# Performance work log

Measured on AMD Instinct MI355X. Metric: run time of the kernel, lower is better.

Reference implementation:

```python
import jax, jax.numpy as jnp
import numpy as np

B, T, D, H = 8, 2048, 1024, 128


def setup_inputs() -> dict:
    key = jax.random.key(0)
    k1, k2, k3, k4 = jax.random.split(key, 4)
    x = jax.random.normal(k1, (B, T, D), dtype=jnp.float32)
    # nn.Linear(D, H, bias=False): y = x @ W.T with W [H, D]; we store W as [D, H]
    Wq = jax.random.normal(k2, (D, H), dtype=jnp.float32) * (1.0 / np.sqrt(D))
    Wk = jax.random.normal(k3, (D, H), dtype=jnp.float32) * (1.0 / np.sqrt(D))
    Wv = jax.random.normal(k4, (D, H), dtype=jnp.float32) * (1.0 / np.sqrt(D))
    return {"x": x, "Wq": Wq, "Wk": Wk, "Wv": Wv}


def reference(x, Wq, Wk, Wv):
    # q, k, v projections (bias-free)
    q = jnp.einsum("btd,dh->bth", x, Wq)
    k = jnp.einsum("btd,dh->bth", x, Wk)
    v = jnp.einsum("btd,dh->bth", x, Wv)
    scale = 1.0 / jnp.sqrt(jnp.asarray(q.shape[-1], dtype=q.dtype))
    # full T x T score matrix, as in the original module
    scores = jnp.einsum("bqh,bkh->bqk", q, k) * scale
    T_ = x.shape[1]
    causal = jnp.tril(jnp.ones((T_, T_), dtype=bool))
    scores = jnp.where(causal[None, :, :], scores, -jnp.inf)
    weights = jax.nn.softmax(scores, axis=-1)
    # dropout is identity in eval mode (deterministic reference)
    return jnp.einsum("bqk,bkh->bqh", weights, v)
```

## Files before the change

kernel.cpp:

```cpp
#include <hip/hip_runtime.h>

typedef float  f32x4  __attribute__((ext_vector_type(4)));
typedef __bf16 bf16x8 __attribute__((ext_vector_type(8)));
typedef unsigned short u16;
typedef unsigned int   u32;
typedef u32 u32x4 __attribute__((ext_vector_type(4)));
typedef u16 u16x4 __attribute__((ext_vector_type(4)));
typedef u16 u16x8 __attribute__((ext_vector_type(8)));
typedef float f32x4v __attribute__((ext_vector_type(4)));

#define B_ 8
#define T_ 2048
#define D_ 1024
#define H_ 128
#define M_ (B_ * T_)

__device__ __forceinline__ u16 f2b(float f) {
  u32 u = __builtin_bit_cast(u32, f);
  u32 r = u + 0x7fffu + ((u >> 16) & 1u);
  return (u16)(r >> 16);
}

__device__ __forceinline__ void gl2lds16(const void* g, void* l) {
  __builtin_amdgcn_global_load_lds(
      (const __attribute__((address_space(1))) void*)g,
      (__attribute__((address_space(3))) void*)l, 16, 0, 0);
}

__global__ __launch_bounds__(256) void wt_kernel(const float* __restrict__ Wq,
                                                 const float* __restrict__ Wk,
                                                 const float* __restrict__ Wv,
                                                 u16* __restrict__ ws) {
  __shared__ u16 Ld[32 * 136];
  const float* W = (blockIdx.y == 0) ? Wq : (blockIdx.y == 1) ? Wk : Wv;
  u16* Wt = ws + (size_t)blockIdx.y * (D_ * H_);
  const int d0 = blockIdx.x * 32;
  const int t = threadIdx.x;
  for (int i = 0; i < 4; ++i) {
    int idx = i * 256 + t;
    int d = idx >> 5, h4 = (idx & 31) * 4;
    f32x4v wv = *(const f32x4v*)(W + (size_t)(d0 + d) * H_ + h4);
    u16x4 bv;
    bv[0] = f2b(wv[0]); bv[1] = f2b(wv[1]); bv[2] = f2b(wv[2]); bv[3] = f2b(wv[3]);
    *(u16x4*)(&Ld[d * 136 + h4]) = bv;
  }
  __syncthreads();
  for (int i = 0; i < 2; ++i) {
    int idx = i * 256 + t;
    int h = idx >> 2, d8 = (idx & 3) * 8;
    u16x8 ov;
    for (int j = 0; j < 8; ++j) ov[j] = Ld[(d8 + j) * 136 + h];
    *(u16x8*)(Wt + (size_t)h * D_ + d0 + d8) = ov;
  }
}

__global__ __launch_bounds__(512, 4) void qkv_gemm(const float* __restrict__ x,
                                                   const u16* __restrict__ Wt_all,
                                                   u16* __restrict__ Qb,
                                                   u16* __restrict__ Kb,
                                                   u16* __restrict__ Vt) {
  __shared__ __attribute__((aligned(16))) u16 As[2][64 * 72];
  __shared__ __attribute__((aligned(16))) u16 Bs[2][192 * 64];
  const int m0 = (int)(blockIdx.x >> 1) * 64;
  const int n0 = (int)(blockIdx.x & 1) * 192;
  const int t = threadIdx.x;
  const int lane = t & 63;
  const int w = t >> 6;
  const int wm = (w & 1) * 32, wn = (w >> 1) * 48;
  const int li = lane & 15, q4 = lane >> 4;
  const int arow = t >> 3, ac0 = (t & 7) * 4;
  const int brr = lane >> 3, bp = lane & 7;

  f32x4 acc[2][3];
  for (int i = 0; i < 2; ++i)
    for (int j = 0; j < 3; ++j) acc[i][j] = (f32x4){0.f, 0.f, 0.f, 0.f};

  f32x4v areg[2];
  auto load_a = [&](int kt) {
    for (int ii = 0; ii < 2; ++ii)
      areg[ii] = *(const f32x4v*)(x + (size_t)(m0 + arow) * D_ + kt * 64 + ac0 + ii * 32);
  };
  auto stage_b = [&](int kt, int sb) {
    for (int s3 = 0; s3 < 3; ++s3) {
      int seg = s3 * 8 + w;
      int r = seg * 8 + brr;
      int u = bp ^ (r & 7);
      gl2lds16(Wt_all + (size_t)(n0 + r) * D_ + kt * 64 + u * 8,
               &Bs[sb][seg * 512]);
    }
  };

  load_a(0);
  stage_b(0, 0);
  for (int kt = 0; kt < 16; ++kt) {
    const int s = kt & 1;
    for (int ii = 0; ii < 2; ++ii) {
      u16x4 av;
      av[0] = f2b(areg[ii][0]); av[1] = f2b(areg[ii][1]);
      av[2] = f2b(areg[ii][2]); av[3] = f2b(areg[ii][3]);
      *(u16x4*)(&As[s][arow * 72 + ac0 + ii * 32]) = av;
    }
    __syncthreads();
    if (kt + 1 < 16) { load_a(kt + 1); stage_b(kt + 1, s ^ 1); }

    for (int kk = 0; kk < 2; ++kk) {
      bf16x8 af[2];
      for (int i = 0; i < 2; ++i)
        af[i] = *(const bf16x8*)(&As[s][(wm + i * 16 + li) * 72 + kk * 32 + q4 * 8]);
      for (int j = 0; j < 3; ++j) {
        int R = wn + j * 16 + li;
        int phys = ((kk << 2) | q4) ^ (R & 7);
        bf16x8 bfr = *(const bf16x8*)(&Bs[s][R * 64 + phys * 8]);
        for (int i = 0; i < 2; ++i)
          acc[i][j] = __builtin_amdgcn_mfma_f32_16x16x32_bf16(af[i], bfr, acc[i][j], 0, 0, 0);
      }
    }
  }

  const float qs = 0.12751740696864213f;
  const int bb = m0 >> 11;
  const int tl0 = (m0 & (T_ - 1)) + wm + q4 * 4;
  for (int j = 0; j < 3; ++j) {
    int n = n0 + wn + j * 16 + li;
    int p = n >> 7, col = n & 127;
    if (p == 2) {
      for (int i = 0; i < 2; ++i) {
        u16x4 pv;
        for (int r = 0; r < 4; ++r) pv[r] = f2b(acc[i][j][r]);
        *(u16x4*)(Vt + (size_t)bb * (H_ * T_) + (size_t)col * T_ + tl0 + i * 16) = pv;
      }
    } else {
      u16* dst = (p == 0) ? Qb : Kb;
      float sc = (p == 0) ? qs : 1.0f;
      for (int i = 0; i < 2; ++i)
        for (int r = 0; r < 4; ++r) {
          int mg = m0 + wm + i * 16 + q4 * 4 + r;
          dst[(size_t)mg * H_ + col] = f2b(acc[i][j][r] * sc);
        }
    }
  }
}

#define NSLOT_PER_B 36

__device__ __forceinline__ int slot_base(int qt) {
  return (qt < 8) ? 2 * (qt - 4) : (qt < 12) ? 8 + 3 * (qt - 8) : 20 + 4 * (qt - 12);
}

__global__ __launch_bounds__(512, 4) void flash_split(const u16* __restrict__ Qb,
                                                      const u16* __restrict__ Kb,
                                                      const u16* __restrict__ Vt,
                                                      float* __restrict__ Opart,
                                                      float* __restrict__ Ls,
                                                      float* __restrict__ out) {
  __shared__ __attribute__((aligned(16))) u16 Ks[2][64 * 128];
  __shared__ __attribute__((aligned(16))) u16 Vs[2][128 * 64];
  __shared__ __attribute__((aligned(16))) u16 Ps[128 * 64];

  int xb = blockIdx.x, qt = 15, split = 0;
  for (int q = 15; q >= 0; --q) {
    int ns = (2 * q + 9) >> 3;
    if (xb < ns) { qt = q; split = xb; break; }
    xb -= ns;
  }
  const int b = blockIdx.y;
  const int nkv = 2 * qt + 2;
  const int nsplit = (2 * qt + 9) >> 3;
  const int kv0t = split * 8;
  const int kv1t = (kv0t + 8 < nkv) ? kv0t + 8 : nkv;
  const int q0 = qt * 128;

  const int t = threadIdx.x;
  const int lane = t & 63;
  const int w = t >> 6;
  const int li = lane & 15, q4 = lane >> 4;

  bf16x8 qf[4];
  const int qrow = b * T_ + q0 + w * 16 + li;
  for (int kk = 0; kk < 4; ++kk)
    qf[kk] = *(const bf16x8*)(Qb + (size_t)qrow * H_ + kk * 32 + q4 * 8);

  f32x4 oacc[8];
  for (int i = 0; i < 8; ++i) oacc[i] = (f32x4){0.f, 0.f, 0.f, 0.f};
  float rs[4] = {0.f, 0.f, 0.f, 0.f};

  auto stage = [&](int jt, int sb) {
    const int j0 = jt * 64;
    for (int i = 0; i < 2; ++i) {
      int seg = i * 8 + w;
      {
        int r = seg * 4 + (lane >> 4);
        int c = (lane & 15) ^ (r & 7);
        gl2lds16(Kb + (size_t)(b * T_ + j0 + r) * H_ + c * 8, &Ks[sb][seg << 9]);
      }
      {
        int r = seg * 8 + (lane >> 3);
        int c = (lane & 7) ^ (r & 7);
        gl2lds16(Vt + (size_t)b * (H_ * T_) + (size_t)r * T_ + j0 + c * 8,
                 &Vs[sb][seg << 9]);
      }
    }
  };

  stage(kv0t, 0);
  for (int jt = kv0t; jt < kv1t; ++jt) {
    const int buf = (jt - kv0t) & 1;
    const int j0 = jt * 64;
    __syncthreads();
    if (jt + 1 < kv1t) stage(jt + 1, buf ^ 1);

    f32x4 sacc[4];
    for (int jn = 0; jn < 4; ++jn) sacc[jn] = (f32x4){0.f, 0.f, 0.f, 0.f};
    for (int jn = 0; jn < 4; ++jn) {
      int row = jn * 16 + li;
      for (int kk = 0; kk < 4; ++kk) {
        int phys = ((kk << 2) | q4) ^ (row & 7);
        bf16x8 kf = *(const bf16x8*)(&Ks[buf][row * 128 + phys * 8]);
        sacc[jn] = __builtin_amdgcn_mfma_f32_16x16x32_bf16(qf[kk], kf, sacc[jn], 0, 0, 0);
      }
    }

    if (jt >= 2 * qt) {
      for (int jn = 0; jn < 4; ++jn) {
        int jg = j0 + jn * 16 + li;
        for (int r = 0; r < 4; ++r) {
          int qg = q0 + w * 16 + q4 * 4 + r;
          if (jg > qg) sacc[jn][r] = -1e30f;
        }
      }
    }

    for (int jn = 0; jn < 4; ++jn)
      for (int r = 0; r < 4; ++r) {
        float p = exp2f(sacc[jn][r]);
        rs[r] += p;
        int row = w * 16 + q4 * 4 + r;
        int col = jn * 16 + li;
        Ps[row * 64 + ((col >> 3) ^ (row & 7)) * 8 + (col & 7)] = f2b(p);
      }

    for (int ks = 0; ks < 2; ++ks) {
      int prow = w * 16 + li;
      int pphys = ((ks << 2) | q4) ^ (prow & 7);
      bf16x8 pa = *(const bf16x8*)(&Ps[prow * 64 + pphys * 8]);
      for (int hn = 0; hn < 8; ++hn) {
        int row = hn * 16 + li;
        int phys = ((ks << 2) | q4) ^ (row & 7);
        bf16x8 vf = *(const bf16x8*)(&Vs[buf][row * 64 + phys * 8]);
        oacc[hn] = __builtin_amdgcn_mfma_f32_16x16x32_bf16(pa, vf, oacc[hn], 0, 0, 0);
      }
    }
  }

  float lr[4];
  for (int r = 0; r < 4; ++r) {
    float s = rs[r];
    for (int off = 1; off < 16; off <<= 1) s += __shfl_xor(s, off, 16);
    lr[r] = s;
  }

  if (nsplit == 1) {
    for (int hn = 0; hn < 8; ++hn)
      for (int r = 0; r < 4; ++r) {
        int qg = b * T_ + q0 + w * 16 + q4 * 4 + r;
        out[(size_t)qg * H_ + hn * 16 + li] = oacc[hn][r] / lr[r];
      }
  } else {
    const int slot = b * NSLOT_PER_B + slot_base(qt) + split;
    float* Od = Opart + (size_t)slot * (128 * 128);
    for (int hn = 0; hn < 8; ++hn)
      for (int r = 0; r < 4; ++r) {
        int qq = w * 16 + q4 * 4 + r;
        Od[qq * 128 + hn * 16 + li] = oacc[hn][r];
      }
    if (li == 0)
      for (int r = 0; r < 4; ++r)
        Ls[slot * 128 + w * 16 + q4 * 4 + r] = lr[r];
  }
}

__global__ __launch_bounds__(512) void flash_merge(const float* __restrict__ Opart,
                                                   const float* __restrict__ Ls,
                                                   float* __restrict__ out) {
  __shared__ float inv_l[128];
  const int qt = 4 + blockIdx.x;
  const int b = blockIdx.y;
  const int nsplit = (2 * qt + 9) >> 3;
  const int slot0 = b * NSLOT_PER_B + slot_base(qt);
  const int t = threadIdx.x;

  if (t < 128) {
    float L = 0.f;
    for (int s = 0; s < nsplit; ++s) L += Ls[(slot0 + s) * 128 + t];
    inv_l[t] = 1.0f / L;
  }
  __syncthreads();

  float* dst = out + ((size_t)b * T_ + (size_t)qt * 128) * H_;
  for (int i = 0; i < 8; ++i) {
    int e4 = i * 512 + t;
    int q = e4 >> 5;
    f32x4 acc = (f32x4){0.f, 0.f, 0.f, 0.f};
    for (int s = 0; s < nsplit; ++s) {
      f32x4 v = *(const f32x4*)(Opart + (size_t)(slot0 + s) * (128 * 128) + e4 * 4);
      acc[0] += v[0]; acc[1] += v[1]; acc[2] += v[2]; acc[3] += v[3];
    }
    float inv = inv_l[q];
    acc[0] *= inv; acc[1] *= inv; acc[2] *= inv; acc[3] *= inv;
    *(f32x4*)(dst + e4 * 4) = acc;
  }
}

extern "C" void kernel_launch(void* const* d_in, const int* in_sizes, int n_in,
                              void* d_out, int out_size, void* d_ws, size_t ws_size,
                              hipStream_t stream) {
  const float* x  = (const float*)d_in[0];
  const float* Wq = (const float*)d_in[1];
  const float* Wk = (const float*)d_in[2];
  const float* Wv = (const float*)d_in[3];
  float* out = (float*)d_out;

  u16* ws = (u16*)d_ws;
  u16* WtAll = ws;
  u16* Qb = ws + 3 * (size_t)(D_ * H_);
  u16* Kb = Qb + (size_t)M_ * H_;
  u16* Vt = Kb + (size_t)M_ * H_;
  float* Opart = (float*)(Vt + (size_t)M_ * H_);
  float* Ls = Opart + (size_t)8 * NSLOT_PER_B * 128 * 128;

  wt_kernel<<<dim3(32, 3), 256, 0, stream>>>(Wq, Wk, Wv, WtAll);
  qkv_gemm<<<dim3(512), 512, 0, stream>>>(x, WtAll, Qb, Kb, Vt);
  flash_split<<<dim3(40, 8), 512, 0, stream>>>(Qb, Kb, Vt, Opart, Ls, out);
  flash_merge<<<dim3(12, 8), 512, 0, stream>>>(Opart, Ls, out);
}
```

Before: 161.7 us.

## Switch flash attention to 32x32 MFMA tiles with finer KV splits

Rewrites the attention kernel to use 32x32x16 bf16 MFMA with 4 waves of 32 query rows each, instead of 8 waves using 16x16x32. It also halves the KV chunk per split from 8 to 4 tiles, producing 72 blocks per batch and more partial slots for the merge kernel. The larger MFMA shape increases operand reuse per LDS read, and the finer split improves load balance across CUs. The cost is higher register pressure from 16-wide accumulators, plus more partial-output traffic and merge work.

```diff
diff --git a/kernel.cpp b/kernel.cpp
--- a/kernel.cpp
+++ b/kernel.cpp
@@ -1,6 +1,7 @@
 #include <hip/hip_runtime.h>
 
 typedef float  f32x4  __attribute__((ext_vector_type(4)));
+typedef float  f32x16 __attribute__((ext_vector_type(16)));
 typedef __bf16 bf16x8 __attribute__((ext_vector_type(8)));
 typedef unsigned short u16;
 typedef unsigned int   u32;
@@ -141,13 +142,15 @@
   }
 }
 
-#define NSLOT_PER_B 36
-
-__device__ __forceinline__ int slot_base(int qt) {
-  return (qt < 8) ? 2 * (qt - 4) : (qt < 12) ? 8 + 3 * (qt - 8) : 20 + 4 * (qt - 12);
-}
-
-__global__ __launch_bounds__(512, 4) void flash_split(const u16* __restrict__ Qb,
+#define NSLOT_PER_B 70
+
+__device__ __forceinline__ int slot_base(int q) {
+  int m = q >> 1;
+  int s = (q & 1) ? m * m : m * (m - 1);
+  return s + q - 2;
+}
+
+__global__ __launch_bounds__(256, 2) void flash_split(const u16* __restrict__ Qb,
                                                       const u16* __restrict__ Kb,
                                                       const u16* __restrict__ Vt,
                                                       float* __restrict__ Opart,
@@ -159,35 +162,37 @@
 
   int xb = blockIdx.x, qt = 15, split = 0;
   for (int q = 15; q >= 0; --q) {
-    int ns = (2 * q + 9) >> 3;
+    int ns = (q >> 1) + 1;
     if (xb < ns) { qt = q; split = xb; break; }
     xb -= ns;
   }
   const int b = blockIdx.y;
   const int nkv = 2 * qt + 2;
-  const int nsplit = (2 * qt + 9) >> 3;
-  const int kv0t = split * 8;
-  const int kv1t = (kv0t + 8 < nkv) ? kv0t + 8 : nkv;
+  const int nsplit = (qt >> 1) + 1;
+  const int kv0t = split * 4;
+  const int kv1t = (kv0t + 4 < nkv) ? kv0t + 4 : nkv;
   const int q0 = qt * 128;
 
   const int t = threadIdx.x;
   const int lane = t & 63;
   const int w = t >> 6;
-  const int li = lane & 15, q4 = lane >> 4;
-
-  bf16x8 qf[4];
-  const int qrow = b * T_ + q0 + w * 16 + li;
-  for (int kk = 0; kk < 4; ++kk)
-    qf[kk] = *(const bf16x8*)(Qb + (size_t)qrow * H_ + kk * 32 + q4 * 8);
-
-  f32x4 oacc[8];
-  for (int i = 0; i < 8; ++i) oacc[i] = (f32x4){0.f, 0.f, 0.f, 0.f};
-  float rs[4] = {0.f, 0.f, 0.f, 0.f};
+  const int l31 = lane & 31, g = lane >> 5;
+
+  bf16x8 qf[8];
+  const int qrow = b * T_ + q0 + w * 32 + l31;
+  for (int kk = 0; kk < 8; ++kk)
+    qf[kk] = *(const bf16x8*)(Qb + (size_t)qrow * H_ + kk * 16 + g * 8);
+
+  f32x16 oacc[4];
+  for (int i = 0; i < 4; ++i)
+    for (int r = 0; r < 16; ++r) oacc[i][r] = 0.f;
+  float rs[16];
+  for (int r = 0; r < 16; ++r) rs[r] = 0.f;
 
   auto stage = [&](int jt, int sb) {
     const int j0 = jt * 64;
-    for (int i = 0; i < 2; ++i) {
-      int seg = i * 8 + w;
+    for (int i = 0; i < 4; ++i) {
+      int seg = i * 4 + w;
       {
         int r = seg * 4 + (lane >> 4);
         int c = (lane & 15) ^ (r & 7);
@@ -209,83 +214,87 @@
     __syncthreads();
     if (jt + 1 < kv1t) stage(jt + 1, buf ^ 1);
 
-    f32x4 sacc[4];
-    for (int jn = 0; jn < 4; ++jn) sacc[jn] = (f32x4){0.f, 0.f, 0.f, 0.f};
-    for (int jn = 0; jn < 4; ++jn) {
-      int row = jn * 16 + li;
-      for (int kk = 0; kk < 4; ++kk) {
-        int phys = ((kk << 2) | q4) ^ (row & 7);
+    f32x16 sacc[2];
+    for (int jn = 0; jn < 2; ++jn)
+      for (int r = 0; r < 16; ++r) sacc[jn][r] = 0.f;
+    for (int jn = 0; jn < 2; ++jn) {
+      int row = jn * 32 + l31;
+      for (int kk = 0; kk < 8; ++kk) {
+        int phys = ((kk << 1) | g) ^ (row & 7);
         bf16x8 kf = *(const bf16x8*)(&Ks[buf][row * 128 + phys * 8]);
-        sacc[jn] = __builtin_amdgcn_mfma_f32_16x16x32_bf16(qf[kk], kf, sacc[jn], 0, 0, 0);
+        sacc[jn] = __builtin_amdgcn_mfma_f32_32x32x16_bf16(qf[kk], kf, sacc[jn], 0, 0, 0);
       }
     }
 
     if (jt >= 2 * qt) {
-      for (int jn = 0; jn < 4; ++jn) {
-        int jg = j0 + jn * 16 + li;
-        for (int r = 0; r < 4; ++r) {
-          int qg = q0 + w * 16 + q4 * 4 + r;
+      for (int jn = 0; jn < 2; ++jn) {
+        int jg = j0 + jn * 32 + l31;
+        for (int r = 0; r < 16; ++r) {
+          int qg = q0 + w * 32 + (r & 3) + 8 * (r >> 2) + 4 * g;
           if (jg > qg) sacc[jn][r] = -1e30f;
         }
       }
     }
 
-    for (int jn = 0; jn < 4; ++jn)
-      for (int r = 0; r < 4; ++r) {
+    for (int jn = 0; jn < 2; ++jn)
+      for (int r = 0; r < 16; ++r) {
         float p = exp2f(sacc[jn][r]);
         rs[r] += p;
-        int row = w * 16 + q4 * 4 + r;
-        int col = jn * 16 + li;
-        Ps[row * 64 + ((col >> 3) ^ (row & 7)) * 8 + (col & 7)] = f2b(p);
-      }
-
-    for (int ks = 0; ks < 2; ++ks) {
-      int prow = w * 16 + li;
-      int pphys = ((ks << 2) | q4) ^ (prow & 7);
-      bf16x8 pa = *(const bf16x8*)(&Ps[prow * 64 + pphys * 8]);
-      for (int hn = 0; hn < 8; ++hn) {
-        int row = hn * 16 + li;
-        int phys = ((ks << 2) | q4) ^ (row & 7);
-        bf16x8 vf = *(const bf16x8*)(&Vs[buf][row * 64 + phys * 8]);
-        oacc[hn] = __builtin_amdgcn_mfma_f32_16x16x32_bf16(pa, vf, oacc[hn], 0, 0, 0);
-      }
-    }
-  }
-
-  float lr[4];
-  for (int r = 0; r < 4; ++r) {
+        int qq = w * 32 + (r & 3) + 8 * (r >> 2) + 4 * g;
+        int jj = jn * 32 + l31;
+        Ps[qq * 64 + (((jj >> 3) ^ (qq & 7)) << 3) + (jj & 7)] = f2b(p);
+      }
+
+    for (int ks = 0; ks < 4; ++ks) {
+      int prow = w * 32 + l31;
+      int punit = ((ks << 1) | g) ^ (prow & 7);
+      bf16x8 pa = *(const bf16x8*)(&Ps[prow * 64 + punit * 8]);
+      for (int hn = 0; hn < 4; ++hn) {
+        int vrow = hn * 32 + l31;
+        int vunit = ((ks << 1) | g) ^ (vrow & 7);
+        bf16x8 vf = *(const bf16x8*)(&Vs[buf][vrow * 64 + vunit * 8]);
+        oacc[hn] = __builtin_amdgcn_mfma_f32_32x32x16_bf16(pa, vf, oacc[hn], 0, 0, 0);
+      }
+    }
+  }
+
+  float lr[16];
+  for (int r = 0; r < 16; ++r) {
     float s = rs[r];
-    for (int off = 1; off < 16; off <<= 1) s += __shfl_xor(s, off, 16);
+    for (int off = 1; off < 32; off <<= 1) s += __shfl_xor(s, off, 32);
     lr[r] = s;
   }
 
   if (nsplit == 1) {
-    for (int hn = 0; hn < 8; ++hn)
-      for (int r = 0; r < 4; ++r) {
-        int qg = b * T_ + q0 + w * 16 + q4 * 4 + r;
-        out[(size_t)qg * H_ + hn * 16 + li] = oacc[hn][r] / lr[r];
+    for (int hn = 0; hn < 4; ++hn)
+      for (int r = 0; r < 16; ++r) {
+        int qq = w * 32 + (r & 3) + 8 * (r >> 2) + 4 * g;
+        int h = hn * 32 + l31;
+        out[(size_t)(b * T_ + q0 + qq) * H_ + h] = oacc[hn][r] / lr[r];
       }
   } else {
     const int slot = b * NSLOT_PER_B + slot_base(qt) + split;
     float* Od = Opart + (size_t)slot * (128 * 128);
-    for (int hn = 0; hn < 8; ++hn)
-      for (int r = 0; r < 4; ++r) {
-        int qq = w * 16 + q4 * 4 + r;
-        Od[qq * 128 + hn * 16 + li] = oacc[hn][r];
-      }
-    if (li == 0)
-      for (int r = 0; r < 4; ++r)
-        Ls[slot * 128 + w * 16 + q4 * 4 + r] = lr[r];
-  }
-}
-
-__global__ __launch_bounds__(512) void flash_merge(const float* __restrict__ Opart,
+    for (int hn = 0; hn < 4; ++hn)
+      for (int r = 0; r < 16; ++r) {
+        int qq = w * 32 + (r & 3) + 8 * (r >> 2) + 4 * g;
+        Od[qq * 128 + hn * 32 + l31] = oacc[hn][r];
+      }
+    if (l31 == 0)
+      for (int r = 0; r < 16; ++r) {
+        int qq = w * 32 + (r & 3) + 8 * (r >> 2) + 4 * g;
+        Ls[slot * 128 + qq] = lr[r];
+      }
+  }
+}
+
+__global__ __launch_bounds__(256) void flash_merge(const float* __restrict__ Opart,
                                                    const float* __restrict__ Ls,
                                                    float* __restrict__ out) {
   __shared__ float inv_l[128];
-  const int qt = 4 + blockIdx.x;
+  const int qt = 2 + blockIdx.x;
   const int b = blockIdx.y;
-  const int nsplit = (2 * qt + 9) >> 3;
+  const int nsplit = (qt >> 1) + 1;
   const int slot0 = b * NSLOT_PER_B + slot_base(qt);
   const int t = threadIdx.x;
 
@@ -297,8 +306,8 @@
   __syncthreads();
 
   float* dst = out + ((size_t)b * T_ + (size_t)qt * 128) * H_;
-  for (int i = 0; i < 8; ++i) {
-    int e4 = i * 512 + t;
+  for (int i = 0; i < 16; ++i) {
+    int e4 = i * 256 + t;
     int q = e4 >> 5;
     f32x4 acc = (f32x4){0.f, 0.f, 0.f, 0.f};
     for (int s = 0; s < nsplit; ++s) {
@@ -330,6 +339,6 @@
 
   wt_kernel<<<dim3(32, 3), 256, 0, stream>>>(Wq, Wk, Wv, WtAll);
   qkv_gemm<<<dim3(512), 512, 0, stream>>>(x, WtAll, Qb, Kb, Vt);
-  flash_split<<<dim3(40, 8), 512, 0, stream>>>(Qb, Kb, Vt, Opart, Ls, out);
-  flash_merge<<<dim3(12, 8), 512, 0, stream>>>(Opart, Ls, out);
-}
+  flash_split<<<dim3(72, 8), 256, 0, stream>>>(Qb, Kb, Vt, Opart, Ls, out);
+  flash_merge<<<dim3(14, 8), 256, 0, stream>>>(Opart, Ls, out);
+}
```

After: 191.3 us. 18.3% more time.

## Retile QKV GEMM per projection and use finer KV splits in flash attention

Applied to the files above, without the earlier changes.

The QKV GEMM tile changes from 64x192 to 64x128, with one projection per blockIdx.y, giving 768 blocks and a higher launch-bounds occupancy target. Each block still reads the x tile, so total reads of x go up. Flash attention now splits KV work into chunks of 6 tiles instead of 8, producing more split blocks (51 per batch) and more merge work with 48 slots. The aim is better load balance and CU fill on the many-CU GPU, at the cost of re-reading x more times and more partial-output traffic.

```diff
diff --git a/kernel.cpp b/kernel.cpp
--- a/kernel.cpp
+++ b/kernel.cpp
@@ -54,26 +54,27 @@
   }
 }
 
-__global__ __launch_bounds__(512, 4) void qkv_gemm(const float* __restrict__ x,
+__global__ __launch_bounds__(512, 6) void qkv_gemm(const float* __restrict__ x,
                                                    const u16* __restrict__ Wt_all,
                                                    u16* __restrict__ Qb,
                                                    u16* __restrict__ Kb,
                                                    u16* __restrict__ Vt) {
   __shared__ __attribute__((aligned(16))) u16 As[2][64 * 72];
-  __shared__ __attribute__((aligned(16))) u16 Bs[2][192 * 64];
-  const int m0 = (int)(blockIdx.x >> 1) * 64;
-  const int n0 = (int)(blockIdx.x & 1) * 192;
+  __shared__ __attribute__((aligned(16))) u16 Bs[2][128 * 64];
+  const int m0 = blockIdx.x * 64;
+  const int n0 = blockIdx.y * 128;
+  const int proj = blockIdx.y;
   const int t = threadIdx.x;
   const int lane = t & 63;
   const int w = t >> 6;
-  const int wm = (w & 1) * 32, wn = (w >> 1) * 48;
+  const int wm = (w & 1) * 32, wn = (w >> 1) * 32;
   const int li = lane & 15, q4 = lane >> 4;
   const int arow = t >> 3, ac0 = (t & 7) * 4;
   const int brr = lane >> 3, bp = lane & 7;
 
-  f32x4 acc[2][3];
+  f32x4 acc[2][2];
   for (int i = 0; i < 2; ++i)
-    for (int j = 0; j < 3; ++j) acc[i][j] = (f32x4){0.f, 0.f, 0.f, 0.f};
+    for (int j = 0; j < 2; ++j) acc[i][j] = (f32x4){0.f, 0.f, 0.f, 0.f};
 
   f32x4v areg[2];
   auto load_a = [&](int kt) {
@@ -81,8 +82,8 @@
       areg[ii] = *(const f32x4v*)(x + (size_t)(m0 + arow) * D_ + kt * 64 + ac0 + ii * 32);
   };
   auto stage_b = [&](int kt, int sb) {
-    for (int s3 = 0; s3 < 3; ++s3) {
-      int seg = s3 * 8 + w;
+    for (int s2 = 0; s2 < 2; ++s2) {
+      int seg = s2 * 8 + w;
       int r = seg * 8 + brr;
       int u = bp ^ (r & 7);
       gl2lds16(Wt_all + (size_t)(n0 + r) * D_ + kt * 64 + u * 8,
@@ -107,7 +108,7 @@
       bf16x8 af[2];
       for (int i = 0; i < 2; ++i)
         af[i] = *(const bf16x8*)(&As[s][(wm + i * 16 + li) * 72 + kk * 32 + q4 * 8]);
-      for (int j = 0; j < 3; ++j) {
+      for (int j = 0; j < 2; ++j) {
         int R = wn + j * 16 + li;
         int phys = ((kk << 2) | q4) ^ (R & 7);
         bf16x8 bfr = *(const bf16x8*)(&Bs[s][R * 64 + phys * 8]);
@@ -120,18 +121,20 @@
   const float qs = 0.12751740696864213f;
   const int bb = m0 >> 11;
   const int tl0 = (m0 & (T_ - 1)) + wm + q4 * 4;
-  for (int j = 0; j < 3; ++j) {
-    int n = n0 + wn + j * 16 + li;
-    int p = n >> 7, col = n & 127;
-    if (p == 2) {
+  if (proj == 2) {
+    for (int j = 0; j < 2; ++j) {
+      int col = wn + j * 16 + li;
       for (int i = 0; i < 2; ++i) {
         u16x4 pv;
         for (int r = 0; r < 4; ++r) pv[r] = f2b(acc[i][j][r]);
         *(u16x4*)(Vt + (size_t)bb * (H_ * T_) + (size_t)col * T_ + tl0 + i * 16) = pv;
       }
-    } else {
-      u16* dst = (p == 0) ? Qb : Kb;
-      float sc = (p == 0) ? qs : 1.0f;
+    }
+  } else {
+    u16* dst = (proj == 0) ? Qb : Kb;
+    const float sc = (proj == 0) ? qs : 1.0f;
+    for (int j = 0; j < 2; ++j) {
+      int col = wn + j * 16 + li;
       for (int i = 0; i < 2; ++i)
         for (int r = 0; r < 4; ++r) {
           int mg = m0 + wm + i * 16 + q4 * 4 + r;
@@ -141,10 +144,15 @@
   }
 }
 
-#define NSLOT_PER_B 36
-
+#define NSLOT_PER_B 48
+
+__device__ __forceinline__ int nsplit_of(int q) { return (2 * q + 7) / 6; }
 __device__ __forceinline__ int slot_base(int qt) {
-  return (qt < 8) ? 2 * (qt - 4) : (qt < 12) ? 8 + 3 * (qt - 8) : 20 + 4 * (qt - 12);
+  int s = 0;
+#pragma unroll
+  for (int q = 3; q < 16; ++q)
+    if (q < qt) s += nsplit_of(q);
+  return s;
 }
 
 __global__ __launch_bounds__(512, 4) void flash_split(const u16* __restrict__ Qb,
@@ -159,15 +167,15 @@
 
   int xb = blockIdx.x, qt = 15, split = 0;
   for (int q = 15; q >= 0; --q) {
-    int ns = (2 * q + 9) >> 3;
+    int ns = nsplit_of(q);
     if (xb < ns) { qt = q; split = xb; break; }
     xb -= ns;
   }
   const int b = blockIdx.y;
   const int nkv = 2 * qt + 2;
-  const int nsplit = (2 * qt + 9) >> 3;
-  const int kv0t = split * 8;
-  const int kv1t = (kv0t + 8 < nkv) ? kv0t + 8 : nkv;
+  const int nsplit = nsplit_of(qt);
+  const int kv0t = split * 6;
+  const int kv1t = (kv0t + 6 < nkv) ? kv0t + 6 : nkv;
   const int q0 = qt * 128;
 
   const int t = threadIdx.x;
@@ -283,9 +291,9 @@
                                                    const float* __restrict__ Ls,
                                                    float* __restrict__ out) {
   __shared__ float inv_l[128];
-  const int qt = 4 + blockIdx.x;
+  const int qt = 3 + blockIdx.x;
   const int b = blockIdx.y;
-  const int nsplit = (2 * qt + 9) >> 3;
+  const int nsplit = nsplit_of(qt);
   const int slot0 = b * NSLOT_PER_B + slot_base(qt);
   const int t = threadIdx.x;
 
@@ -329,7 +337,7 @@
   float* Ls = Opart + (size_t)8 * NSLOT_PER_B * 128 * 128;
 
   wt_kernel<<<dim3(32, 3), 256, 0, stream>>>(Wq, Wk, Wv, WtAll);
-  qkv_gemm<<<dim3(512), 512, 0, stream>>>(x, WtAll, Qb, Kb, Vt);
-  flash_split<<<dim3(40, 8), 512, 0, stream>>>(Qb, Kb, Vt, Opart, Ls, out);
-  flash_merge<<<dim3(12, 8), 512, 0, stream>>>(Opart, Ls, out);
-}
+  qkv_gemm<<<dim3(256, 3), 512, 0, stream>>>(x, WtAll, Qb, Kb, Vt);
+  flash_split<<<dim3(51, 8), 512, 0, stream>>>(Qb, Kb, Vt, Opart, Ls, out);
+  flash_merge<<<dim3(13, 8), 512, 0, stream>>>(Opart, Ls, out);
+}
```

Result: no change. 164.0 us (+1.4%).

## Fuse split-KV merge into flash kernel via atomic last-block counter, finer splits

Applied to the files above, without the earlier changes.

Drops the separate merge kernel launch. The last split block of each query tile, found with an atomic counter after a threadfence, now performs the reduction and normalization. The KV chunk per split shrinks from 8 to 5 tiles, which raises the grid from 320 to 488 blocks for better load balance across CUs. The cost is more partial-output traffic and merge work, plus a memset launch to clear the counters.

```diff
diff --git a/kernel.cpp b/kernel.cpp
--- a/kernel.cpp
+++ b/kernel.cpp
@@ -141,10 +141,16 @@
   }
 }
 
-#define NSLOT_PER_B 36
-
+#define CHUNK 5
+#define NSLOT_PER_B 59
+
+__device__ __forceinline__ int nsplit_of(int q) { return (2 * q + 6) / 5; }
 __device__ __forceinline__ int slot_base(int qt) {
-  return (qt < 8) ? 2 * (qt - 4) : (qt < 12) ? 8 + 3 * (qt - 8) : 20 + 4 * (qt - 12);
+  int s = 0;
+#pragma unroll
+  for (int q = 2; q < 16; ++q)
+    if (q < qt) s += nsplit_of(q);
+  return s;
 }
 
 __global__ __launch_bounds__(512, 4) void flash_split(const u16* __restrict__ Qb,
@@ -152,6 +158,7 @@
                                                       const u16* __restrict__ Vt,
                                                       float* __restrict__ Opart,
                                                       float* __restrict__ Ls,
+                                                      int* __restrict__ Cnt,
                                                       float* __restrict__ out) {
   __shared__ __attribute__((aligned(16))) u16 Ks[2][64 * 128];
   __shared__ __attribute__((aligned(16))) u16 Vs[2][128 * 64];
@@ -159,15 +166,15 @@
 
   int xb = blockIdx.x, qt = 15, split = 0;
   for (int q = 15; q >= 0; --q) {
-    int ns = (2 * q + 9) >> 3;
+    int ns = nsplit_of(q);
     if (xb < ns) { qt = q; split = xb; break; }
     xb -= ns;
   }
   const int b = blockIdx.y;
   const int nkv = 2 * qt + 2;
-  const int nsplit = (2 * qt + 9) >> 3;
-  const int kv0t = split * 8;
-  const int kv1t = (kv0t + 8 < nkv) ? kv0t + 8 : nkv;
+  const int nsplit = nsplit_of(qt);
+  const int kv0t = split * CHUNK;
+  const int kv1t = (kv0t + CHUNK < nkv) ? kv0t + CHUNK : nkv;
   const int q0 = qt * 128;
 
   const int t = threadIdx.x;
@@ -265,49 +272,51 @@
         int qg = b * T_ + q0 + w * 16 + q4 * 4 + r;
         out[(size_t)qg * H_ + hn * 16 + li] = oacc[hn][r] / lr[r];
       }
-  } else {
-    const int slot = b * NSLOT_PER_B + slot_base(qt) + split;
-    float* Od = Opart + (size_t)slot * (128 * 128);
-    for (int hn = 0; hn < 8; ++hn)
-      for (int r = 0; r < 4; ++r) {
-        int qq = w * 16 + q4 * 4 + r;
-        Od[qq * 128 + hn * 16 + li] = oacc[hn][r];
-      }
-    if (li == 0)
-      for (int r = 0; r < 4; ++r)
-        Ls[slot * 128 + w * 16 + q4 * 4 + r] = lr[r];
-  }
-}
-
-__global__ __launch_bounds__(512) void flash_merge(const float* __restrict__ Opart,
-                                                   const float* __restrict__ Ls,
-                                                   float* __restrict__ out) {
-  __shared__ float inv_l[128];
-  const int qt = 4 + blockIdx.x;
-  const int b = blockIdx.y;
-  const int nsplit = (2 * qt + 9) >> 3;
+    return;
+  }
+
   const int slot0 = b * NSLOT_PER_B + slot_base(qt);
-  const int t = threadIdx.x;
-
-  if (t < 128) {
-    float L = 0.f;
-    for (int s = 0; s < nsplit; ++s) L += Ls[(slot0 + s) * 128 + t];
-    inv_l[t] = 1.0f / L;
-  }
+  const int slot = slot0 + split;
+  float* Od = Opart + (size_t)slot * (128 * 128);
+  for (int hn = 0; hn < 8; ++hn)
+    for (int r = 0; r < 4; ++r) {
+      int qq = w * 16 + q4 * 4 + r;
+      Od[qq * 128 + hn * 16 + li] = oacc[hn][r];
+    }
+  if (li == 0)
+    for (int r = 0; r < 4; ++r)
+      Ls[slot * 128 + w * 16 + q4 * 4 + r] = lr[r];
+
+  __threadfence();
   __syncthreads();
-
-  float* dst = out + ((size_t)b * T_ + (size_t)qt * 128) * H_;
-  for (int i = 0; i < 8; ++i) {
-    int e4 = i * 512 + t;
-    int q = e4 >> 5;
-    f32x4 acc = (f32x4){0.f, 0.f, 0.f, 0.f};
-    for (int s = 0; s < nsplit; ++s) {
-      f32x4 v = *(const f32x4*)(Opart + (size_t)(slot0 + s) * (128 * 128) + e4 * 4);
-      acc[0] += v[0]; acc[1] += v[1]; acc[2] += v[2]; acc[3] += v[3];
-    }
-    float inv = inv_l[q];
-    acc[0] *= inv; acc[1] *= inv; acc[2] *= inv; acc[3] *= inv;
-    *(f32x4*)(dst + e4 * 4) = acc;
+  volatile int* lastflag = (volatile int*)Ps;
+  if (t == 0) {
+    int old = atomicAdd(&Cnt[b * 16 + qt], 1);
+    *lastflag = (old == nsplit - 1) ? 1 : 0;
+  }
+  __syncthreads();
+  if (*lastflag) {
+    __threadfence();
+    float* inv_l = (float*)(Ps + 256);
+    if (t < 128) {
+      float L = 0.f;
+      for (int s = 0; s < nsplit; ++s) L += Ls[(slot0 + s) * 128 + t];
+      inv_l[t] = 1.0f / L;
+    }
+    __syncthreads();
+    float* dst = out + ((size_t)b * T_ + (size_t)qt * 128) * H_;
+    for (int i = 0; i < 8; ++i) {
+      int e4 = i * 512 + t;
+      int q = e4 >> 5;
+      f32x4 acc = (f32x4){0.f, 0.f, 0.f, 0.f};
+      for (int s = 0; s < nsplit; ++s) {
+        f32x4 v = *(const f32x4*)(Opart + (size_t)(slot0 + s) * (128 * 128) + e4 * 4);
+        acc[0] += v[0]; acc[1] += v[1]; acc[2] += v[2]; acc[3] += v[3];
+      }
+      float inv = inv_l[q];
+      acc[0] *= inv; acc[1] *= inv; acc[2] *= inv; acc[3] *= inv;
+      *(f32x4*)(dst + e4 * 4) = acc;
+    }
   }
 }
 
@@ -327,9 +336,10 @@
   u16* Vt = Kb + (size_t)M_ * H_;
   float* Opart = (float*)(Vt + (size_t)M_ * H_);
   float* Ls = Opart + (size_t)8 * NSLOT_PER_B * 128 * 128;
-
+  int* Cnt = (int*)(Ls + (size_t)8 * NSLOT_PER_B * 128);
+
+  hipMemsetAsync(Cnt, 0, 8 * 16 * sizeof(int), stream);
   wt_kernel<<<dim3(32, 3), 256, 0, stream>>>(Wq, Wk, Wv, WtAll);
   qkv_gemm<<<dim3(512), 512, 0, stream>>>(x, WtAll, Qb, Kb, Vt);
-  flash_split<<<dim3(40, 8), 512, 0, stream>>>(Qb, Kb, Vt, Opart, Ls, out);
-  flash_merge<<<dim3(12, 8), 512, 0, stream>>>(Opart, Ls, out);
-}
+  flash_split<<<dim3(61, 8), 512, 0, stream>>>(Qb, Kb, Vt, Opart, Ls, Cnt, out);
+}
```

Result: slower. 319.9 us (+97.9%).
